# Performance work log

Hardware: AMD Instinct MI355X
Metric: run time of the kernel (lower is better)

The kernel has to match this reference:

```python
import jax, jax.numpy as jnp
import numpy as np

B, L, D = 2, 2048, 1024
H = 16
DH = D // H
FACTOR = 0.6
U = max(1, min(L, int(FACTOR * L)))  # 1228 selected queries


def setup_inputs() -> dict:
    key = jax.random.key(0)
    ks = jax.random.split(key, 9)
    s = 0.02
    return {
        "x": jax.random.normal(ks[0], (B, L, D), dtype=jnp.float32),
        "Wq": jax.random.normal(ks[1], (D, D), dtype=jnp.float32) * s,
        "bq": jnp.zeros((D,), dtype=jnp.float32),
        "Wk": jax.random.normal(ks[2], (D, D), dtype=jnp.float32) * s,
        "bk": jnp.zeros((D,), dtype=jnp.float32),
        "Wv": jax.random.normal(ks[3], (D, D), dtype=jnp.float32) * s,
        "bv": jnp.zeros((D,), dtype=jnp.float32),
        "Wo": jax.random.normal(ks[4], (D, D), dtype=jnp.float32) * s,
        "bo": jnp.zeros((D,), dtype=jnp.float32),
    }


def _split_heads(x):
    b, l, d = x.shape
    return x.reshape(b, l, H, DH).transpose(0, 2, 1, 3)  # [b,h,l,dh]


def reference(x, Wq, bq, Wk, bk, Wv, bv, Wo, bo):
    b, l, _ = x.shape
    scale = 1.0 / jnp.sqrt(jnp.asarray(DH, dtype=x.dtype))

    q = _split_heads(x @ Wq + bq)  # [b,h,l,dh]
    k = _split_heads(x @ Wk + bk)
    v = _split_heads(x @ Wv + bv)

    # full scores for sparsity heuristic
    scores = jnp.einsum("bhqd,bhkd->bhqk", q, k) * scale  # [b,h,l,l]
    sparsity = scores.max(axis=-1) - scores.mean(axis=-1)  # [b,h,l]

    _, top_idx = jax.lax.top_k(sparsity, U)  # [b,h,U]

    # gather selected queries, attend only on those rows
    q_sel = jnp.take_along_axis(q, top_idx[..., None], axis=2)  # [b,h,U,dh]
    scores_sel = jnp.einsum("bhud,bhkd->bhuk", q_sel, k) * scale  # [b,h,U,l]
    attn = jax.nn.softmax(scores_sel, axis=-1)
    out_sel = jnp.einsum("bhuk,bhkd->bhud", attn, v)  # [b,h,U,dh]

    # scatter back into zero-initialized output
    bi = jnp.arange(b)[:, None, None]
    hi = jnp.arange(H)[None, :, None]
    out = jnp.zeros_like(q).at[bi, hi, top_idx].set(out_sel)  # [b,h,l,dh]

    out = out.transpose(0, 2, 1, 3).reshape(b, l, D)
    return out @ Wo + bo
```

## Files before the change

kernel.cpp:

```cpp
#include <hip/hip_runtime.h>
#include <math.h>
#include <stdint.h>

#define Bn 2
#define Ln 2048
#define Dn 1024
#define Hn 16
#define DHn 64
#define Un 1228
#define BHn (Bn*Hn)
#define SCALE 0.125f
#define WIN 32
#define WHALF 16
#define SXf 16.0f
#define SWf 256.0f
#define SQf 16.0f
#define SVf 16.0f
#define SPf 16.0f
#define ESC_PROJ (1.0f / 4096.0f)
#define ESC_OUT  (1.0f / 65536.0f)
#define PSC (SCALE / 256.0f)
#define QPS 88

typedef _Float16 f16;
typedef __attribute__((ext_vector_type(8))) _Float16 f16x8;
typedef __attribute__((ext_vector_type(4))) float f32x4;
struct h4s { f16 x, y, z, w; };

__device__ __forceinline__ void splitf16(float f, f16& hi, f16& lo) {
  hi = (f16)f;
  lo = (f16)(f - (float)hi);
}

__device__ __forceinline__ void gl_lds16(const void* g, void* l) {
  __builtin_amdgcn_global_load_lds(
      (const __attribute__((address_space(1))) void*)g,
      (__attribute__((address_space(3))) void*)l, 16, 0, 0);
}

#define MFMA(a, b, c) __builtin_amdgcn_mfma_f32_16x16x32_f16((a), (b), (c), 0, 0, 0)

__global__ __launch_bounds__(256) void split_kernel(
    const float* __restrict__ in, f16* __restrict__ oh, f16* __restrict__ ol, int n4) {
  int i = blockIdx.x * 256 + threadIdx.x;
  if (i >= n4) return;
  float4 v = ((const float4*)in)[i];
  h4s h, l;
  splitf16(v.x * SXf, h.x, l.x); splitf16(v.y * SXf, h.y, l.y);
  splitf16(v.z * SXf, h.z, l.z); splitf16(v.w * SXf, h.w, l.w);
  ((h4s*)oh)[i] = h; ((h4s*)ol)[i] = l;
}

__global__ __launch_bounds__(256) void tsplit_w4(
    const float* __restrict__ W0, const float* __restrict__ W1,
    const float* __restrict__ W2, const float* __restrict__ W3,
    f16* __restrict__ oh, f16* __restrict__ ol) {
  __shared__ float ts[64][65];
  const int t = threadIdx.x;
  const int r0 = blockIdx.x * 64, c0 = blockIdx.y * 64;
  const int z = blockIdx.z;
  const float* in = (z == 0) ? W0 : (z == 1) ? W1 : (z == 2) ? W2 : W3;
#pragma unroll
  for (int c = 0; c < 4; ++c) {
    int f = (c * 256 + t) * 4; int row = f >> 6, col = f & 63;
    float4 v = *(const float4*)&in[(size_t)(r0 + row) * Dn + c0 + col];
    ts[row][col] = v.x; ts[row][col + 1] = v.y; ts[row][col + 2] = v.z; ts[row][col + 3] = v.w;
  }
  __syncthreads();
#pragma unroll
  for (int c = 0; c < 4; ++c) {
    int f = (c * 256 + t) * 4; int crow = f >> 6, rcol = f & 63;
    h4s h, l;
    splitf16(ts[rcol + 0][crow] * SWf, h.x, l.x);
    splitf16(ts[rcol + 1][crow] * SWf, h.y, l.y);
    splitf16(ts[rcol + 2][crow] * SWf, h.z, l.z);
    splitf16(ts[rcol + 3][crow] * SWf, h.w, l.w);
    size_t o = (size_t)(z * 1024 + c0 + crow) * Dn + r0 + rcol;
    *(h4s*)&oh[o] = h; *(h4s*)&ol[o] = l;
  }
}

__global__ void gemm_qkv(
    const f16* __restrict__ Ah, const f16* __restrict__ Al,
    const f16* __restrict__ Bth, const f16* __restrict__ Btl,
    const float* __restrict__ bq, const float* __restrict__ bk, const float* __restrict__ bv,
    f16* __restrict__ Qbh, f16* __restrict__ Qbl,
    f16* __restrict__ Kbh, f16* __restrict__ Kbl,
    f16* __restrict__ Vh16, int K) {
  __shared__ f16 sAh[128 * 32], sAl[128 * 32], sBh[128 * 32], sBl[128 * 32];
  const int t = threadIdx.x;
  const int w = t >> 6, lane = t & 63, lm = lane & 15, q = lane >> 4;
  const int wr = w >> 1, wc = w & 1;
  const int n0 = blockIdx.x * 128, m0 = blockIdx.y * 128;
  f32x4 acc[4][4] = {};
  for (int k0 = 0; k0 < K; k0 += 32) {
    const f16* s0 = Ah + (size_t)m0 * K + k0;
    const f16* s1 = Al + (size_t)m0 * K + k0;
    const f16* s2 = Bth + (size_t)n0 * K + k0;
    const f16* s3 = Btl + (size_t)n0 * K + k0;
#pragma unroll
    for (int c = 0; c < 2; ++c) {
      int f = (c * 256 + t) * 8; int row = f >> 5, col = f & 31;
      size_t go = (size_t)row * K + col;
      gl_lds16(s0 + go, &sAh[f]);
      gl_lds16(s1 + go, &sAl[f]);
      gl_lds16(s2 + go, &sBh[f]);
      gl_lds16(s3 + go, &sBl[f]);
    }
    __syncthreads();
    f16x8 a_h[4], a_l[4], b_h[4], b_l[4];
#pragma unroll
    for (int mi = 0; mi < 4; ++mi) {
      int r = (wr * 64 + mi * 16 + lm) * 32 + q * 8;
      a_h[mi] = *(const f16x8*)&sAh[r];
      a_l[mi] = *(const f16x8*)&sAl[r];
    }
#pragma unroll
    for (int ni = 0; ni < 4; ++ni) {
      int r = (wc * 64 + ni * 16 + lm) * 32 + q * 8;
      b_h[ni] = *(const f16x8*)&sBh[r];
      b_l[ni] = *(const f16x8*)&sBl[r];
    }
#pragma unroll
    for (int mi = 0; mi < 4; ++mi)
#pragma unroll
      for (int ni = 0; ni < 4; ++ni) {
        acc[mi][ni] = MFMA(a_h[mi], b_h[ni], acc[mi][ni]);
        acc[mi][ni] = MFMA(a_h[mi], b_l[ni], acc[mi][ni]);
        acc[mi][ni] = MFMA(a_l[mi], b_h[ni], acc[mi][ni]);
      }
    __syncthreads();
  }
#pragma unroll
  for (int mi = 0; mi < 4; ++mi)
#pragma unroll
    for (int ni = 0; ni < 4; ++ni) {
      int nglob = n0 + wc * 64 + ni * 16;
      int seg = nglob >> 10;
      int c = (nglob & 1023) + lm;
      const float* bp = (seg == 0) ? bq : (seg == 1) ? bk : bv;
      float bvv = bp[c];
#pragma unroll
      for (int r = 0; r < 4; ++r) {
        int grow = m0 + wr * 64 + mi * 16 + q * 4 + r;
        float v = acc[mi][ni][r] * ESC_PROJ + bvv;
        size_t o = (size_t)grow * 1024 + c;
        if (seg == 0) {
          f16 hh, ll; splitf16(v * SQf, hh, ll); Qbh[o] = hh; Qbl[o] = ll;
        } else if (seg == 1) {
          f16 hh, ll; splitf16(v * SQf, hh, ll); Kbh[o] = hh; Kbl[o] = ll;
        } else {
          Vh16[o] = (f16)(v * SVf);
        }
      }
    }
}

__global__ __launch_bounds__(256) void tsplit_v(
    const f16* __restrict__ Vh16, f16* __restrict__ out) {
  __shared__ f16 ts[64][72];
  const int t = threadIdx.x;
  const int l0 = blockIdx.x * 64;
  const int bh = blockIdx.y, b = bh >> 4, h = bh & 15;
#pragma unroll
  for (int c = 0; c < 2; ++c) {
    int e = c * 256 + t; int row = e >> 3, cg = e & 7;
    *(uint4*)&ts[row][cg * 8] =
        *(const uint4*)&Vh16[((size_t)b * Ln + l0 + row) * Dn + h * DHn + cg * 8];
  }
  __syncthreads();
#pragma unroll
  for (int c = 0; c < 2; ++c) {
    int e = c * 256 + t; int drow = e >> 3, lg = e & 7;
    f16 tmp[8];
#pragma unroll
    for (int j = 0; j < 8; ++j) tmp[j] = ts[lg * 8 + j][drow];
    *(uint4*)&out[((size_t)bh * DHn + drow) * Ln + l0 + lg * 8] = *(uint4*)tmp;
  }
}

__global__ __launch_bounds__(256, 4) void gemm_a1(
    const f16* __restrict__ A,
    const f16* __restrict__ Bth, const f16* __restrict__ Btl,
    const float* __restrict__ bias, float escale,
    float* __restrict__ Cf, int M, int N, int K) {
  __shared__ f16 sA[128 * 32], sBh[64 * 32], sBl[64 * 32];
  const int t = threadIdx.x;
  const int w = t >> 6, lane = t & 63, lm = lane & 15, q = lane >> 4;
  const int wr = w >> 1, wc = w & 1;
  int ob = blockIdx.x;
  int wg = (ob & 7) * 64 + (ob >> 3);
  const int n0 = (wg & 15) * 64, m0 = (wg >> 4) * 128;
  f32x4 acc[4][2] = {};
  for (int k0 = 0; k0 < K; k0 += 32) {
    const f16* s0 = A + (size_t)m0 * K + k0;
    const f16* s2 = Bth + (size_t)n0 * K + k0;
    const f16* s3 = Btl + (size_t)n0 * K + k0;
#pragma unroll
    for (int c = 0; c < 2; ++c) {
      int f = (c * 256 + t) * 8; int row = f >> 5, col = f & 31;
      gl_lds16(s0 + (size_t)row * K + col, &sA[f]);
    }
    {
      int f = t * 8; int row = f >> 5, col = f & 31;
      gl_lds16(s2 + (size_t)row * K + col, &sBh[f]);
      gl_lds16(s3 + (size_t)row * K + col, &sBl[f]);
    }
    __syncthreads();
    f16x8 a_[4], b_h[2], b_l[2];
#pragma unroll
    for (int mi = 0; mi < 4; ++mi)
      a_[mi] = *(const f16x8*)&sA[(wr * 64 + mi * 16 + lm) * 32 + q * 8];
#pragma unroll
    for (int ni = 0; ni < 2; ++ni) {
      int r = (wc * 32 + ni * 16 + lm) * 32 + q * 8;
      b_h[ni] = *(const f16x8*)&sBh[r];
      b_l[ni] = *(const f16x8*)&sBl[r];
    }
#pragma unroll
    for (int mi = 0; mi < 4; ++mi)
#pragma unroll
      for (int ni = 0; ni < 2; ++ni) {
        acc[mi][ni] = MFMA(a_[mi], b_h[ni], acc[mi][ni]);
        acc[mi][ni] = MFMA(a_[mi], b_l[ni], acc[mi][ni]);
      }
    __syncthreads();
  }
#pragma unroll
  for (int mi = 0; mi < 4; ++mi)
#pragma unroll
    for (int ni = 0; ni < 2; ++ni) {
      int gcol = n0 + wc * 32 + ni * 16 + lm;
      float bvv = bias[gcol];
#pragma unroll
      for (int r = 0; r < 4; ++r) {
        int grow = m0 + wr * 64 + mi * 16 + q * 4 + r;
        Cf[(size_t)grow * N + gcol] = acc[mi][ni][r] * escale + bvv;
      }
    }
}

__global__ __launch_bounds__(256) void ksum_part(
    const f16* __restrict__ Kh, float* __restrict__ ksum) {
  __shared__ float red[4][64];
  const int t = threadIdx.x, d = t & 63, seg = t >> 6;
  const int bx = blockIdx.x, bh = blockIdx.y, b = bh >> 4, h = bh & 15;
  float s = 0.f;
  const int lbase = bx * 256 + seg * 64;
  for (int r = 0; r < 64; ++r) {
    size_t o = ((size_t)b * Ln + lbase + r) * Dn + h * DHn + d;
    s += (float)Kh[o];
  }
  red[seg][d] = s;
  __syncthreads();
  if (t < 64) atomicAdd(&ksum[bh * DHn + t], red[0][t] + red[1][t] + red[2][t] + red[3][t]);
}

__global__ __launch_bounds__(256, 2) void attn_stats_mfma(
    const f16* __restrict__ Qh, const f16* __restrict__ Kh,
    const float* __restrict__ ksum,
    float* __restrict__ row_max, float* __restrict__ spars) {
  __shared__ f16 sQh[128 * 64], sKh[2][128 * 64];
  __shared__ float redm[128][5];
  const int t = threadIdx.x;
  const int w = t >> 6, lane = t & 63, lm = lane & 15, q = lane >> 4;
  const int bh = blockIdx.y, b = bh >> 4, h = bh & 15;
  const int q0 = blockIdx.x * 128;
  const f16* qsh = Qh + ((size_t)b * Ln + q0) * Dn + h * DHn;
  const f16* kbase = Kh + (size_t)b * Ln * Dn + h * DHn;
#pragma unroll
  for (int c = 0; c < 4; ++c) {
    int f = (c * 256 + t) * 8; int row = f >> 6, c16 = (f >> 3) & 7;
    size_t go = (size_t)row * Dn + ((c16 ^ (row & 7)) << 3);
    gl_lds16(qsh + go, &sQh[f]);
    gl_lds16(kbase + go, &sKh[0][f]);
  }
  asm volatile("s_waitcnt vmcnt(0)" ::: "memory");
  __builtin_amdgcn_s_barrier();
  f16x8 a_h[8][2];
#pragma unroll
  for (int mi = 0; mi < 8; ++mi)
#pragma unroll
    for (int ks = 0; ks < 2; ++ks) {
      int row = mi * 16 + lm;
      int r = row * 64 + (((ks * 4 + q) ^ (row & 7)) << 3);
      a_h[mi][ks] = *(const f16x8*)&sQh[r];
    }
  float rmax[8][4];
#pragma unroll
  for (int mi = 0; mi < 8; ++mi)
#pragma unroll
    for (int r = 0; r < 4; ++r) rmax[mi][r] = -1e30f;

  for (int kt = 0; kt < Ln / 128; ++kt) {
    const int cur = kt & 1;
    if (kt < Ln / 128 - 1) {
      const f16* ksh = kbase + (size_t)(kt + 1) * 128 * Dn;
#pragma unroll
      for (int c = 0; c < 4; ++c) {
        int f = (c * 256 + t) * 8; int row = f >> 6, c16 = (f >> 3) & 7;
        size_t go = (size_t)row * Dn + ((c16 ^ (row & 7)) << 3);
        gl_lds16(ksh + go, &sKh[cur ^ 1][f]);
      }
    }
#pragma unroll
    for (int ni = 0; ni < 2; ++ni) {
      int bcol = (w * 2 + ni) * 16;
      f16x8 b_h[2];
#pragma unroll
      for (int ks = 0; ks < 2; ++ks) {
        int row = bcol + lm;
        int r = row * 64 + (((ks * 4 + q) ^ (row & 7)) << 3);
        b_h[ks] = *(const f16x8*)&sKh[cur][r];
      }
#pragma unroll
      for (int mi = 0; mi < 8; ++mi) {
        f32x4 acc = {0.f, 0.f, 0.f, 0.f};
        __builtin_amdgcn_s_setprio(1);
        acc = MFMA(a_h[mi][0], b_h[0], acc);
        acc = MFMA(a_h[mi][1], b_h[1], acc);
        __builtin_amdgcn_s_setprio(0);
#pragma unroll
        for (int r = 0; r < 4; ++r) rmax[mi][r] = fmaxf(rmax[mi][r], acc[r]);
      }
    }
    asm volatile("s_waitcnt vmcnt(0) lgkmcnt(0)" ::: "memory");
    __builtin_amdgcn_s_barrier();
  }
#pragma unroll
  for (int mi = 0; mi < 8; ++mi)
#pragma unroll
    for (int r = 0; r < 4; ++r) {
      float v = rmax[mi][r];
      v = fmaxf(v, __shfl_xor(v, 1)); v = fmaxf(v, __shfl_xor(v, 2));
      v = fmaxf(v, __shfl_xor(v, 4)); v = fmaxf(v, __shfl_xor(v, 8));
      if (lm == 0) redm[mi * 16 + q * 4 + r][w] = v;
    }
  __syncthreads();
  if (t < 128) {
    float m = fmaxf(fmaxf(redm[t][0], redm[t][1]), fmaxf(redm[t][2], redm[t][3]));
    float dot = 0.f;
    const float* kp = ksum + bh * DHn;
#pragma unroll
    for (int d = 0; d < 64; ++d) {
      int idx = t * 64 + ((((d >> 3) ^ (t & 7)) << 3) | (d & 7));
      dot += (float)sQh[idx] * kp[d];
    }
    row_max[(size_t)bh * Ln + q0 + t] = m * PSC;
    spars[(size_t)bh * Ln + q0 + t] = m * PSC - dot * (PSC / (float)Ln);
  }
}

__global__ __launch_bounds__(1024) void topk_sort(
    const float* __restrict__ spars, int* __restrict__ top_idx, int* __restrict__ wrow) {
  __shared__ unsigned long long keys[Ln];
  const int t = threadIdx.x;
  const int bh = blockIdx.x;
  for (int i = t; i < Ln; i += 1024) {
    unsigned u = __float_as_uint(spars[(size_t)bh * Ln + i]);
    u = (u & 0x80000000u) ? ~u : (u | 0x80000000u);
    u = ~u;
    keys[i] = ((unsigned long long)u << 32) | (unsigned)i;
  }
  __syncthreads();
  for (int k = 2; k <= Ln; k <<= 1) {
    for (int j = k >> 1; j > 0; j >>= 1) {
      int i = ((t & ~(j - 1)) << 1) | (t & (j - 1));
      int ixj = i | j;
      unsigned long long a = keys[i], bb = keys[ixj];
      bool up = ((i & k) == 0);
      if ((a > bb) == up) { keys[i] = bb; keys[ixj] = a; }
      __syncthreads();
    }
  }
  for (int u = t; u < Un - WHALF; u += 1024)
    top_idx[(size_t)bh * Un + u] = (int)(keys[u] & 0xFFFFFFFFu);
  if (t < WIN) wrow[bh * WIN + t] = (int)(keys[Un - WHALF + t] & 0xFFFFFFFFu);
}

__global__ __launch_bounds__(256) void refine_part(
    const f16* __restrict__ Qbh, const f16* __restrict__ Qbl,
    const f16* __restrict__ Kbh, const f16* __restrict__ Kbl,
    const int* __restrict__ wrow,
    float* __restrict__ pmaxf, float* __restrict__ psum) {
  __shared__ float qs[WIN][68];
  __shared__ float redm[4][WIN], reds[4][WIN];
  const int t = threadIdx.x;
  const int bx = blockIdx.x, bh = blockIdx.y, b = bh >> 4, h = bh & 15;
  {
    int j = t >> 3, d0 = (t & 7) * 8;
    int qi = wrow[bh * WIN + j];
    size_t o = ((size_t)b * Ln + qi) * Dn + h * DHn + d0;
    f16x8 vh = *(const f16x8*)&Qbh[o];
    f16x8 vl = *(const f16x8*)&Qbl[o];
#pragma unroll
    for (int e = 0; e < 8; ++e) qs[j][d0 + e] = (float)vh[e] + (float)vl[e];
  }
  __syncthreads();
  const int ki = bx * 256 + t;
  const size_t ko = ((size_t)b * Ln + ki) * Dn + h * DHn;
  float s[WIN];
#pragma unroll
  for (int j = 0; j < WIN; ++j) s[j] = 0.f;
  for (int d0 = 0; d0 < 64; d0 += 8) {
    f16x8 vh = *(const f16x8*)&Kbh[ko + d0];
    f16x8 vl = *(const f16x8*)&Kbl[ko + d0];
    float kf[8];
#pragma unroll
    for (int e = 0; e < 8; ++e) kf[e] = (float)vh[e] + (float)vl[e];
#pragma unroll
    for (int e = 0; e < 8; ++e)
#pragma unroll
      for (int j = 0; j < WIN; ++j)
        s[j] = fmaf(kf[e], qs[j][d0 + e], s[j]);
  }
  const int w = t >> 6, lane = t & 63;
#pragma unroll
  for (int j = 0; j < WIN; ++j) {
    float mx = s[j], sm = s[j];
#pragma unroll
    for (int off = 1; off < 64; off <<= 1) {
      mx = fmaxf(mx, __shfl_xor(mx, off));
      sm += __shfl_xor(sm, off);
    }
    if (lane == 0) { redm[w][j] = mx; reds[w][j] = sm; }
  }
  __syncthreads();
  if (t < WIN) {
    float mx = fmaxf(fmaxf(redm[0][t], redm[1][t]), fmaxf(redm[2][t], redm[3][t]));
    float sm = reds[0][t] + reds[1][t] + reds[2][t] + reds[3][t];
    size_t o = ((size_t)bh * WIN + t) * 8 + bx;
    pmaxf[o] = mx;
    psum[o] = sm;
  }
}

__global__ __launch_bounds__(64) void topk_final(
    const float* __restrict__ pmaxf, const float* __restrict__ psum,
    const int* __restrict__ wrow, int* __restrict__ top_idx) {
  __shared__ float spxL[WIN];
  const int bh = blockIdx.x;
  const int t = threadIdx.x;
  if (t < WIN) {
    float m = -1e30f, s = 0.f;
#pragma unroll
    for (int p = 0; p < 8; ++p) {
      size_t o = ((size_t)bh * WIN + t) * 8 + p;
      m = fmaxf(m, pmaxf[o]);
      s += psum[o];
    }
    spxL[t] = PSC * (m - s * (1.0f / (float)Ln));
  }
  __syncthreads();
  if (t != 0) return;
  float v[WIN]; int r[WIN];
#pragma unroll
  for (int j = 0; j < WIN; ++j) { v[j] = spxL[j]; r[j] = wrow[bh * WIN + j]; }
  unsigned taken = 0;
  for (int s2 = 0; s2 < WHALF; ++s2) {
    int best = -1;
    for (int j = 0; j < WIN; ++j) {
      if (taken & (1u << j)) continue;
      if (best < 0 || v[j] > v[best] || (v[j] == v[best] && r[j] < r[best])) best = j;
    }
    taken |= 1u << best;
    top_idx[(size_t)bh * Un + (Un - WHALF) + s2] = r[best];
  }
}

__global__ __launch_bounds__(256, 3) void attn_sel_part(
    const f16* __restrict__ Qh, const f16* __restrict__ Kh,
    const f16* __restrict__ Vth,
    const int* __restrict__ topi, const float* __restrict__ row_max,
    float* __restrict__ pO, float* __restrict__ pD) {
  __shared__ f16 sK[2][64 * 64], sV[2][64 * 64];
  __shared__ f16 sQP[64 * QPS];
  __shared__ float rmL[64];
  __shared__ int qxL[64];
  __shared__ float dred[64][5];
  const int t = threadIdx.x;
  const int w = t >> 6, lane = t & 63, lm = lane & 15, q = lane >> 4;
  const int half = blockIdx.y & 1, bh = blockIdx.y >> 1, b = bh >> 4, h = bh & 15;
  const int u0 = blockIdx.x * 64;
  const int nrows = (Un - u0 < 64) ? (Un - u0) : 64;
  if (t < 64) {
    int qi = topi[(size_t)bh * Un + ((t < nrows) ? (u0 + t) : 0)];
    qxL[t] = qi;
    rmL[t] = row_max[(size_t)bh * Ln + qi];
  }
  __syncthreads();
#pragma unroll
  for (int c = 0; c < 2; ++c) {
    int f = (c * 256 + t) * 8; int row = f >> 6, col = f & 63;
    size_t go = ((size_t)b * Ln + qxL[row]) * Dn + h * DHn + col;
    *(uint4*)&sQP[row * QPS + col] = *(const uint4*)&Qh[go];
  }
  __syncthreads();
  f16x8 aq[4][2];
#pragma unroll
  for (int mi = 0; mi < 4; ++mi)
#pragma unroll
    for (int ks = 0; ks < 2; ++ks)
      aq[mi][ks] = *(const f16x8*)&sQP[(mi * 16 + lm) * QPS + ks * 32 + q * 8];
  f32x4 oacc[4] = {};
  float dacc[4][4] = {};

  const f16* kbase = Kh + (size_t)b * Ln * Dn + h * DHn;
  const f16* vbase = Vth + (size_t)bh * DHn * Ln;

  {
    const int l0 = half * 1024;
#pragma unroll
    for (int c = 0; c < 2; ++c) {
      int f = (c * 256 + t) * 8; int row = f >> 6, c16 = (f >> 3) & 7;
      int sc = (c16 ^ (row & 7)) << 3;
      gl_lds16(kbase + (size_t)(l0 + row) * Dn + sc, &sK[0][f]);
      gl_lds16(vbase + (size_t)row * Ln + l0 + sc, &sV[0][f]);
    }
  }
  asm volatile("s_waitcnt vmcnt(0) lgkmcnt(0)" ::: "memory");
  __builtin_amdgcn_s_barrier();

  for (int kt = 0; kt < 16; ++kt) {
    const int cur = kt & 1;
    f16x8 kb[2];
#pragma unroll
    for (int ks = 0; ks < 2; ++ks) {
      int row = w * 16 + lm;
      kb[ks] = *(const f16x8*)&sK[cur][row * 64 + (((ks * 4 + q) ^ (row & 7)) << 3)];
    }
    if (kt < 15) {
      const int ln0 = half * 1024 + (kt + 1) * 64;
#pragma unroll
      for (int c = 0; c < 2; ++c) {
        int f = (c * 256 + t) * 8; int row = f >> 6, c16 = (f >> 3) & 7;
        int sc = (c16 ^ (row & 7)) << 3;
        gl_lds16(kbase + (size_t)(ln0 + row) * Dn + sc, &sK[cur ^ 1][f]);
        gl_lds16(vbase + (size_t)row * Ln + ln0 + sc, &sV[cur ^ 1][f]);
      }
    }
#pragma unroll
    for (int mi = 0; mi < 4; ++mi) {
      f32x4 acc = {0.f, 0.f, 0.f, 0.f};
      __builtin_amdgcn_s_setprio(1);
      acc = MFMA(aq[mi][0], kb[0], acc);
      acc = MFMA(aq[mi][1], kb[1], acc);
      __builtin_amdgcn_s_setprio(0);
#pragma unroll
      for (int r = 0; r < 4; ++r) {
        int row = mi * 16 + q * 4 + r;
        float p = __expf(acc[r] * PSC - rmL[row]);
        dacc[mi][r] += p;
        sQP[row * QPS + w * 16 + lm] = (f16)(p * SPf);
      }
    }
    asm volatile("s_waitcnt lgkmcnt(0)" ::: "memory");
    __builtin_amdgcn_s_barrier();
    f16x8 vb[2];
#pragma unroll
    for (int ks = 0; ks < 2; ++ks) {
      int row = w * 16 + lm;
      vb[ks] = *(const f16x8*)&sV[cur][row * 64 + (((ks * 4 + q) ^ (row & 7)) << 3)];
    }
#pragma unroll
    for (int mi = 0; mi < 4; ++mi) {
      f16x8 pf0 = *(const f16x8*)&sQP[(mi * 16 + lm) * QPS + 0 * 32 + q * 8];
      f16x8 pf1 = *(const f16x8*)&sQP[(mi * 16 + lm) * QPS + 1 * 32 + q * 8];
      __builtin_amdgcn_s_setprio(1);
      oacc[mi] = MFMA(pf0, vb[0], oacc[mi]);
      oacc[mi] = MFMA(pf1, vb[1], oacc[mi]);
      __builtin_amdgcn_s_setprio(0);
    }
    asm volatile("s_waitcnt vmcnt(0)" ::: "memory");
    __builtin_amdgcn_s_barrier();
  }
#pragma unroll
  for (int mi = 0; mi < 4; ++mi)
#pragma unroll
    for (int r = 0; r < 4; ++r) {
      float v = dacc[mi][r];
      v += __shfl_xor(v, 1); v += __shfl_xor(v, 2);
      v += __shfl_xor(v, 4); v += __shfl_xor(v, 8);
      if (lm == 0) dred[mi * 16 + q * 4 + r][w] = v;
    }
  __syncthreads();
  const size_t pbase = ((size_t)half * BHn + bh) * 1280 + u0;
  if (t < 64)
    pD[pbase + t] = dred[t][0] + dred[t][1] + dred[t][2] + dred[t][3];
#pragma unroll
  for (int mi = 0; mi < 4; ++mi)
#pragma unroll
    for (int r = 0; r < 4; ++r) {
      int row = mi * 16 + q * 4 + r;
      pO[(pbase + row) * 64 + w * 16 + lm] = oacc[mi][r];
    }
}

__global__ __launch_bounds__(256) void attn_combine(
    const float* __restrict__ pO, const float* __restrict__ pD,
    const int* __restrict__ topi, f16* __restrict__ AOh) {
  const int t = threadIdx.x;
  const int u0 = blockIdx.x * 64, bh = blockIdx.y, b = bh >> 4, h = bh & 15;
  const int nrows = (Un - u0 < 64) ? (Un - u0) : 64;
  const int row = t >> 2, pg = t & 3;
  if (row >= nrows) return;
  int qi = topi[(size_t)bh * Un + u0 + row];
  size_t i0 = (size_t)bh * 1280 + u0 + row;
  size_t i1 = (size_t)BHn * 1280 + i0;
  float dinv = 1.0f / (pD[i0] + pD[i1]);
  const float* p0 = &pO[i0 * 64 + pg * 16];
  const float* p1 = &pO[i1 * 64 + pg * 16];
  f16 buf[16];
#pragma unroll
  for (int c = 0; c < 4; ++c) {
    float4 a = *(const float4*)&p0[c * 4];
    float4 bb = *(const float4*)&p1[c * 4];
    buf[c * 4 + 0] = (f16)((a.x + bb.x) * dinv);
    buf[c * 4 + 1] = (f16)((a.y + bb.y) * dinv);
    buf[c * 4 + 2] = (f16)((a.z + bb.z) * dinv);
    buf[c * 4 + 3] = (f16)((a.w + bb.w) * dinv);
  }
  f16* dst = &AOh[((size_t)b * Ln + qi) * Dn + h * DHn + pg * 16];
  *(uint4*)&dst[0] = *(uint4*)&buf[0];
  *(uint4*)&dst[8] = *(uint4*)&buf[8];
}

extern "C" void kernel_launch(void* const* d_in, const int* in_sizes, int n_in,
                              void* d_out, int out_size, void* d_ws, size_t ws_size,
                              hipStream_t stream) {
  (void)in_sizes; (void)n_in; (void)out_size; (void)ws_size;
  const float* x  = (const float*)d_in[0];
  const float* Wq = (const float*)d_in[1];
  const float* bq = (const float*)d_in[2];
  const float* Wk = (const float*)d_in[3];
  const float* bk = (const float*)d_in[4];
  const float* Wv = (const float*)d_in[5];
  const float* bv = (const float*)d_in[6];
  const float* Wo = (const float*)d_in[7];
  const float* bo = (const float*)d_in[8];
  float* out = (float*)d_out;

  uint8_t* p = (uint8_t*)d_ws;
  const size_t NE = (size_t)Bn * Ln * Dn;
  f16* xh = (f16*)p;  p += NE * 2;
  f16* xl = (f16*)p;  p += NE * 2;
  f16* Wt_h = (f16*)p; p += (size_t)4096 * Dn * 2;
  f16* Wt_l = (f16*)p; p += (size_t)4096 * Dn * 2;
  f16* Qbh = (f16*)p; p += NE * 2;
  f16* Qbl = (f16*)p; p += NE * 2;
  f16* Kbh = (f16*)p; p += NE * 2;
  f16* Kbl = (f16*)p; p += NE * 2;
  f16* Vh16 = (f16*)p; p += NE * 2;
  f16* Vth  = (f16*)p; p += NE * 2;
  float* rowmax = (float*)p; p += (size_t)BHn * Ln * 4;
  float* spars  = (float*)p; p += (size_t)BHn * Ln * 4;
  float* ksum   = (float*)p; p += (size_t)BHn * DHn * 4;
  int* topi     = (int*)p;   p += (size_t)BHn * Un * 4;
  int* wrow     = (int*)p;   p += (size_t)BHn * WIN * 4;
  float* pmaxf  = (float*)p; p += (size_t)BHn * WIN * 8 * 4;
  float* psum   = (float*)p; p += (size_t)BHn * WIN * 8 * 4;
  float* pD     = (float*)p; p += (size_t)2 * BHn * 1280 * 4;
  float* pO     = (float*)p; p += (size_t)2 * BHn * 1280 * 64 * 4;
  f16* AOh = xh;

  dim3 blk(256);
  hipLaunchKernelGGL(split_kernel, dim3((int)(NE / 4 / 256)), blk, 0, stream, x, xh, xl, (int)(NE / 4));
  hipLaunchKernelGGL(tsplit_w4, dim3(16, 16, 4), blk, 0, stream, Wq, Wk, Wv, Wo, Wt_h, Wt_l);
  hipLaunchKernelGGL(gemm_qkv, dim3(24, 32), blk, 0, stream, xh, xl, Wt_h, Wt_l,
                     bq, bk, bv, Qbh, Qbl, Kbh, Kbl, Vh16, Dn);
  hipLaunchKernelGGL(tsplit_v, dim3(Ln / 64, BHn), blk, 0, stream, Vh16, Vth);
  hipMemsetAsync(ksum, 0, (size_t)BHn * DHn * 4, stream);
  hipLaunchKernelGGL(ksum_part, dim3(8, BHn), blk, 0, stream, Kbh, ksum);
  hipLaunchKernelGGL(attn_stats_mfma, dim3(Ln / 128, BHn), blk, 0, stream,
                     Qbh, Kbh, ksum, rowmax, spars);
  hipLaunchKernelGGL(topk_sort, dim3(BHn), dim3(1024), 0, stream, spars, topi, wrow);
  hipLaunchKernelGGL(refine_part, dim3(8, BHn), blk, 0, stream,
                     Qbh, Qbl, Kbh, Kbl, wrow, pmaxf, psum);
  hipLaunchKernelGGL(topk_final, dim3(BHn), dim3(64), 0, stream, pmaxf, psum, wrow, topi);
  hipMemsetAsync(AOh, 0, NE * 2, stream);
  hipLaunchKernelGGL(attn_sel_part, dim3((Un + 63) / 64, 2 * BHn), blk, 0, stream,
                     Qbh, Kbh, Vth, topi, rowmax, pO, pD);
  hipLaunchKernelGGL(attn_combine, dim3((Un + 63) / 64, BHn), blk, 0, stream,
                     pO, pD, topi, AOh);
  hipLaunchKernelGGL(gemm_a1, dim3(512), blk, 0, stream, AOh,
                     Wt_h + (size_t)3072 * Dn, Wt_l + (size_t)3072 * Dn, bo,
                     ESC_OUT, out, Bn * Ln, Dn, Dn);
}
```

Before: 375.2 us.

## Double-buffer LDS tiles in QKV and output projection GEMMs

Both projection GEMMs now keep two LDS buffers and issue the global-to-LDS loads for the next K tile before running the MFMAs on the current tile. This lets memory latency overlap with compute and cuts the loop to one barrier per iteration instead of two. The cost is doubled LDS use: 64KB for gemm_qkv and 32KB per block for gemm_a1, which asks for 4 blocks per CU. That may lower occupancy and offset the overlap.

Result: slower. 395.5 us (+5.4%).

```diff
diff --git a/kernel.cpp b/kernel.cpp
--- a/kernel.cpp
+++ b/kernel.cpp
@@ -80,6 +80,20 @@
   }
 }
 
+#define QKV_STAGE_TILE(BUF, KOFF) do { \
+    const f16* s0_ = Ah + (size_t)m0 * K + (KOFF); \
+    const f16* s1_ = Al + (size_t)m0 * K + (KOFF); \
+    const f16* s2_ = Bth + (size_t)n0 * K + (KOFF); \
+    const f16* s3_ = Btl + (size_t)n0 * K + (KOFF); \
+    _Pragma("unroll") for (int c_ = 0; c_ < 2; ++c_) { \
+      int f_ = (c_ * 256 + t) * 8; int row_ = f_ >> 5, col_ = f_ & 31; \
+      size_t go_ = (size_t)row_ * K + col_; \
+      gl_lds16(s0_ + go_, &sAh[BUF][f_]); \
+      gl_lds16(s1_ + go_, &sAl[BUF][f_]); \
+      gl_lds16(s2_ + go_, &sBh[BUF][f_]); \
+      gl_lds16(s3_ + go_, &sBl[BUF][f_]); \
+    } } while (0)
+
 __global__ void gemm_qkv(
     const f16* __restrict__ Ah, const f16* __restrict__ Al,
     const f16* __restrict__ Bth, const f16* __restrict__ Btl,
@@ -87,39 +101,30 @@
     f16* __restrict__ Qbh, f16* __restrict__ Qbl,
     f16* __restrict__ Kbh, f16* __restrict__ Kbl,
     f16* __restrict__ Vh16, int K) {
-  __shared__ f16 sAh[128 * 32], sAl[128 * 32], sBh[128 * 32], sBl[128 * 32];
+  __shared__ f16 sAh[2][128 * 32], sAl[2][128 * 32], sBh[2][128 * 32], sBl[2][128 * 32];
   const int t = threadIdx.x;
   const int w = t >> 6, lane = t & 63, lm = lane & 15, q = lane >> 4;
   const int wr = w >> 1, wc = w & 1;
   const int n0 = blockIdx.x * 128, m0 = blockIdx.y * 128;
   f32x4 acc[4][4] = {};
+  QKV_STAGE_TILE(0, 0);
+  asm volatile("s_waitcnt vmcnt(0)" ::: "memory");
+  __builtin_amdgcn_s_barrier();
   for (int k0 = 0; k0 < K; k0 += 32) {
-    const f16* s0 = Ah + (size_t)m0 * K + k0;
-    const f16* s1 = Al + (size_t)m0 * K + k0;
-    const f16* s2 = Bth + (size_t)n0 * K + k0;
-    const f16* s3 = Btl + (size_t)n0 * K + k0;
-#pragma unroll
-    for (int c = 0; c < 2; ++c) {
-      int f = (c * 256 + t) * 8; int row = f >> 5, col = f & 31;
-      size_t go = (size_t)row * K + col;
-      gl_lds16(s0 + go, &sAh[f]);
-      gl_lds16(s1 + go, &sAl[f]);
-      gl_lds16(s2 + go, &sBh[f]);
-      gl_lds16(s3 + go, &sBl[f]);
-    }
-    __syncthreads();
+    const int cur = (k0 >> 5) & 1;
+    if (k0 + 32 < K) QKV_STAGE_TILE(cur ^ 1, k0 + 32);
     f16x8 a_h[4], a_l[4], b_h[4], b_l[4];
 #pragma unroll
     for (int mi = 0; mi < 4; ++mi) {
       int r = (wr * 64 + mi * 16 + lm) * 32 + q * 8;
-      a_h[mi] = *(const f16x8*)&sAh[r];
-      a_l[mi] = *(const f16x8*)&sAl[r];
+      a_h[mi] = *(const f16x8*)&sAh[cur][r];
+      a_l[mi] = *(const f16x8*)&sAl[cur][r];
     }
 #pragma unroll
     for (int ni = 0; ni < 4; ++ni) {
       int r = (wc * 64 + ni * 16 + lm) * 32 + q * 8;
-      b_h[ni] = *(const f16x8*)&sBh[r];
-      b_l[ni] = *(const f16x8*)&sBl[r];
+      b_h[ni] = *(const f16x8*)&sBh[cur][r];
+      b_l[ni] = *(const f16x8*)&sBl[cur][r];
     }
 #pragma unroll
     for (int mi = 0; mi < 4; ++mi)
@@ -129,7 +134,8 @@
         acc[mi][ni] = MFMA(a_h[mi], b_l[ni], acc[mi][ni]);
         acc[mi][ni] = MFMA(a_l[mi], b_h[ni], acc[mi][ni]);
       }
-    __syncthreads();
+    asm volatile("s_waitcnt vmcnt(0) lgkmcnt(0)" ::: "memory");
+    __builtin_amdgcn_s_barrier();
   }
 #pragma unroll
   for (int mi = 0; mi < 4; ++mi)
@@ -179,12 +185,24 @@
   }
 }
 
+#define A1_STAGE_TILE(BUF, KOFF) do { \
+    const f16* s0_ = A + (size_t)m0 * K + (KOFF); \
+    const f16* s2_ = Bth + (size_t)n0 * K + (KOFF); \
+    const f16* s3_ = Btl + (size_t)n0 * K + (KOFF); \
+    _Pragma("unroll") for (int c_ = 0; c_ < 2; ++c_) { \
+      int f_ = (c_ * 256 + t) * 8; int row_ = f_ >> 5, col_ = f_ & 31; \
+      gl_lds16(s0_ + (size_t)row_ * K + col_, &sA[BUF][f_]); \
+    } \
+    { int f_ = t * 8; int row_ = f_ >> 5, col_ = f_ & 31; \
+      gl_lds16(s2_ + (size_t)row_ * K + col_, &sBh[BUF][f_]); \
+      gl_lds16(s3_ + (size_t)row_ * K + col_, &sBl[BUF][f_]); } } while (0)
+
 __global__ __launch_bounds__(256, 4) void gemm_a1(
     const f16* __restrict__ A,
     const f16* __restrict__ Bth, const f16* __restrict__ Btl,
     const float* __restrict__ bias, float escale,
     float* __restrict__ Cf, int M, int N, int K) {
-  __shared__ f16 sA[128 * 32], sBh[64 * 32], sBl[64 * 32];
+  __shared__ f16 sA[2][128 * 32], sBh[2][64 * 32], sBl[2][64 * 32];
   const int t = threadIdx.x;
   const int w = t >> 6, lane = t & 63, lm = lane & 15, q = lane >> 4;
   const int wr = w >> 1, wc = w & 1;
@@ -192,30 +210,21 @@
   int wg = (ob & 7) * 64 + (ob >> 3);
   const int n0 = (wg & 15) * 64, m0 = (wg >> 4) * 128;
   f32x4 acc[4][2] = {};
+  A1_STAGE_TILE(0, 0);
+  asm volatile("s_waitcnt vmcnt(0)" ::: "memory");
+  __builtin_amdgcn_s_barrier();
   for (int k0 = 0; k0 < K; k0 += 32) {
-    const f16* s0 = A + (size_t)m0 * K + k0;
-    const f16* s2 = Bth + (size_t)n0 * K + k0;
-    const f16* s3 = Btl + (size_t)n0 * K + k0;
-#pragma unroll
-    for (int c = 0; c < 2; ++c) {
-      int f = (c * 256 + t) * 8; int row = f >> 5, col = f & 31;
-      gl_lds16(s0 + (size_t)row * K + col, &sA[f]);
-    }
-    {
-      int f = t * 8; int row = f >> 5, col = f & 31;
-      gl_lds16(s2 + (size_t)row * K + col, &sBh[f]);
-      gl_lds16(s3 + (size_t)row * K + col, &sBl[f]);
-    }
-    __syncthreads();
+    const int cur = (k0 >> 5) & 1;
+    if (k0 + 32 < K) A1_STAGE_TILE(cur ^ 1, k0 + 32);
     f16x8 a_[4], b_h[2], b_l[2];
 #pragma unroll
     for (int mi = 0; mi < 4; ++mi)
-      a_[mi] = *(const f16x8*)&sA[(wr * 64 + mi * 16 + lm) * 32 + q * 8];
+      a_[mi] = *(const f16x8*)&sA[cur][(wr * 64 + mi * 16 + lm) * 32 + q * 8];
 #pragma unroll
     for (int ni = 0; ni < 2; ++ni) {
       int r = (wc * 32 + ni * 16 + lm) * 32 + q * 8;
-      b_h[ni] = *(const f16x8*)&sBh[r];
-      b_l[ni] = *(const f16x8*)&sBl[r];
+      b_h[ni] = *(const f16x8*)&sBh[cur][r];
+      b_l[ni] = *(const f16x8*)&sBl[cur][r];
     }
 #pragma unroll
     for (int mi = 0; mi < 4; ++mi)
@@ -224,7 +233,8 @@
         acc[mi][ni] = MFMA(a_[mi], b_h[ni], acc[mi][ni]);
         acc[mi][ni] = MFMA(a_[mi], b_l[ni], acc[mi][ni]);
       }
-    __syncthreads();
+    asm volatile("s_waitcnt vmcnt(0) lgkmcnt(0)" ::: "memory");
+    __builtin_amdgcn_s_barrier();
   }
 #pragma unroll
   for (int mi = 0; mi < 4; ++mi)
```
